# Optimization experiments

Measured on AMD Instinct MI355X. Metric: run time of the kernel, lower is better.

## Reference

```python
import jax, jax.numpy as jnp
import numpy as np

EPS_NORM = 1e-12  # F.normalize default eps
EPS_LN = 1e-6     # LayerNorm eps from module


def setup_inputs() -> dict:
    key = jax.random.key(0)
    ks = jax.random.split(key, 4)
    bs, S, h = 32, 512, 1024
    data = jax.random.normal(ks[0], (bs, S, h), dtype=jnp.float32)
    scale = 1.0 / np.sqrt(h)
    wq = jax.random.normal(ks[1], (h, h), dtype=jnp.float32) * scale
    wk = jax.random.normal(ks[2], (h, h), dtype=jnp.float32) * scale
    wv = jax.random.normal(ks[3], (h, h), dtype=jnp.float32) * scale
    gamma = jnp.ones((h,), dtype=jnp.float32)
    beta = jnp.zeros((h,), dtype=jnp.float32)
    return {"data": data, "wq": wq, "wk": wk, "wv": wv, "gamma": gamma, "beta": beta}


def reference(data, wq, wk, wv, gamma, beta):
    # data: [bs, S, h]; single-head attention, dropout is identity in eval mode
    bs, S, h = data.shape
    temperature = jnp.asarray(h, data.dtype) ** 0.5
    # torch Linear: x @ W^T
    q = jnp.einsum('bsh,dh->bsd', data, wq)
    k = jnp.einsum('bsh,dh->bsd', data, wk)
    v = jnp.einsum('bsh,dh->bsd', data, wv)
    # scaled scores [bs, S, S]
    attn = jnp.einsum('bsd,btd->bst', q / temperature, k)
    # divide by abs of the GLOBAL min over the whole tensor
    attn = attn / jnp.abs(jnp.min(attn))
    # L2-normalize along last dim (F.normalize)
    l2 = jnp.sqrt(jnp.sum(attn * attn, axis=-1, keepdims=True))
    attn = attn / jnp.maximum(l2, EPS_NORM)
    attn = jax.nn.softmax(attn, axis=-1)
    out = jnp.einsum('bst,btd->bsd', attn, v)
    out = out + data  # residual
    # LayerNorm over last dim
    mean = jnp.mean(out, axis=-1, keepdims=True)
    var = jnp.mean((out - mean) ** 2, axis=-1, keepdims=True)
    out = (out - mean) * jax.lax.rsqrt(var + EPS_LN) * gamma + beta
    # concat flattened output [bs, S*h] with flattened attn [bs, S*S]
    return jnp.concatenate((out.reshape(bs, -1), attn.reshape(bs, -1)), axis=1)
```

## Files before the change

### kernel.cpp

```cpp
#include <hip/hip_runtime.h>
#include <hip/hip_bf16.h>


typedef float f32x4 __attribute__((ext_vector_type(4)));
typedef int i32x4v __attribute__((ext_vector_type(4)));
typedef int i32x8v __attribute__((ext_vector_type(8)));

struct alignas(16) US8 { unsigned short s[8]; };
struct alignas(8)  US4 { unsigned short s[4]; };

#define WS_XB   0ull
#define WS_XF8  33554432ull
#define WS_WF8  50331648ull
#define WS_QF8  53477376ull
#define WS_KF8  70254592ull
#define WS_VT8  87031808ull
#define WS_S    103809024ull
#define WS_P8   120586240ull
#define WS_O    128974848ull
#define WS_NEED 162529280ull

__device__ __forceinline__ unsigned short f32_to_bf16(float f) {
  unsigned int u = __builtin_bit_cast(unsigned int, f);
  u += 0x7fffu + ((u >> 16) & 1u);
  return (unsigned short)(u >> 16);
}
__device__ __forceinline__ float bf16_to_f32(unsigned short h) {
  return __builtin_bit_cast(float, (unsigned int)h << 16);
}

__device__ __forceinline__ void gload_lds16(const void* g, void* lds) {
  __builtin_amdgcn_global_load_lds(
      (const __attribute__((address_space(1))) unsigned int*)g,
      (__attribute__((address_space(3))) unsigned int*)lds, 16, 0, 0);
}

__device__ __forceinline__ float wave_sum(float v) {
#pragma unroll
  for (int off = 32; off > 0; off >>= 1) v += __shfl_xor(v, off);
  return v;
}
__device__ __forceinline__ float wave_max(float v) {
#pragma unroll
  for (int off = 32; off > 0; off >>= 1) v = fmaxf(v, __shfl_xor(v, off));
  return v;
}

__device__ __forceinline__ unsigned int pk_fp8x4(float a, float b, float c, float d) {
  unsigned int v = 0;
  v = __builtin_amdgcn_cvt_pk_fp8_f32(a, b, v, false);
  v = __builtin_amdgcn_cvt_pk_fp8_f32(c, d, v, true);
  return v;
}
__device__ __forceinline__ unsigned char f32_to_fp8(float v) {
  return (unsigned char)(__builtin_amdgcn_cvt_pk_fp8_f32(v, v, 0, false) & 0xffu);
}

__global__ __launch_bounds__(256) void cvt_data(const float* __restrict__ src,
                                                unsigned short* __restrict__ dstb,
                                                unsigned int* __restrict__ dst8,
                                                int n8) {
  int i = blockIdx.x * 256 + threadIdx.x;
  if (i >= n8) return;
  const float4* sp = (const float4*)(src + (size_t)i * 8);
  float4 a = sp[0], b = sp[1];
  US8 u;
  u.s[0] = f32_to_bf16(a.x); u.s[1] = f32_to_bf16(a.y);
  u.s[2] = f32_to_bf16(a.z); u.s[3] = f32_to_bf16(a.w);
  u.s[4] = f32_to_bf16(b.x); u.s[5] = f32_to_bf16(b.y);
  u.s[6] = f32_to_bf16(b.z); u.s[7] = f32_to_bf16(b.w);
  *(US8*)(dstb + (size_t)i * 8) = u;
  uint2 w;
  w.x = pk_fp8x4(a.x, a.y, a.z, a.w);
  w.y = pk_fp8x4(b.x, b.y, b.z, b.w);
  *(uint2*)(dst8 + (size_t)i * 2) = w;
}

__global__ __launch_bounds__(256) void cvt_w3(const float* __restrict__ wq,
                                              const float* __restrict__ wk,
                                              const float* __restrict__ wv,
                                              unsigned int* __restrict__ dst8) {
  const int z = blockIdx.y;
  const float* src = (z == 0) ? wq : (z == 1) ? wk : wv;
  int i = blockIdx.x * 256 + threadIdx.x;
  const float4* sp = (const float4*)(src + (size_t)i * 8);
  float4 a = sp[0], b = sp[1];
  uint2 w;
  w.x = pk_fp8x4(a.x, a.y, a.z, a.w);
  w.y = pk_fp8x4(b.x, b.y, b.z, b.w);
  *(uint2*)(dst8 + (size_t)z * 262144 + (size_t)i * 2) = w;
}

template <int KB, int NKT>
__device__ __forceinline__ void f8c128(const char* __restrict__ Ag,
                                       const char* __restrict__ Bg,
                                       char* lds, f32x4 (&acc)[4][4]) {
  const int tid = threadIdx.x;
  const int w = tid >> 6, lane = tid & 63;
  const int wm = w >> 1, wn = w & 1;
  const int lr = lane & 15, lk4 = lane >> 4;

  const int sc = ((tid & 3) ^ ((tid >> 3) & 3)) * 16;
  const char* pA = Ag + (size_t)(tid >> 2) * KB + sc;
  const char* pB = Bg + (size_t)(tid >> 2) * KB + sc;
  const size_t R64 = (size_t)64 * KB;

  const int swz = (lr >> 1) & 3;
  const int c0 = (lk4 & 1) * 2;
  const int cb0 = ((c0) ^ swz) * 16;
  const int cb1 = ((c0 + 1) ^ swz) * 16;
  const int panA = (lk4 >> 1) * 8192;
  const int panB = 16384 + (lk4 >> 1) * 8192;
  const int rowA = (wm * 64 + lr) * 64;
  const int rowB = (wn * 64 + lr) * 64;

#define STAGE8(DD)                                                            \
  do {                                                                        \
    char* dd_ = (DD);                                                         \
    gload_lds16(pA,            dd_ + tid * 16);                               \
    gload_lds16(pA + R64,      dd_ + 4096 + tid * 16);                        \
    gload_lds16(pA + 64,       dd_ + 8192 + tid * 16);                        \
    gload_lds16(pA + R64 + 64, dd_ + 12288 + tid * 16);                       \
    gload_lds16(pB,            dd_ + 16384 + tid * 16);                       \
    gload_lds16(pB + R64,      dd_ + 20480 + tid * 16);                       \
    gload_lds16(pB + 64,       dd_ + 24576 + tid * 16);                       \
    gload_lds16(pB + R64 + 64, dd_ + 28672 + tid * 16);                       \
    pA += 128; pB += 128;                                                     \
  } while (0)

#define MK8(D, OFF)                                                           \
  do {                                                                        \
    i32x4v lo_ = *(const i32x4v*)(sp + (OFF) + cb0);                          \
    i32x4v hi_ = *(const i32x4v*)(sp + (OFF) + cb1);                          \
    D[0] = lo_[0]; D[1] = lo_[1]; D[2] = lo_[2]; D[3] = lo_[3];               \
    D[4] = hi_[0]; D[5] = hi_[1]; D[6] = hi_[2]; D[7] = hi_[3];               \
  } while (0)

#define MFMA128(ACC, AV, BV)                                                  \
  asm("v_mfma_f32_16x16x128_f8f6f4 %0, %1, %2, %0"                            \
      : "+a"(ACC) : "v"(AV), "v"(BV))

  STAGE8(lds);

#pragma unroll
  for (int t = 0; t < NKT; ++t) {
    const int slot = t & 1;
    if (t + 1 < NKT) {
      STAGE8(lds + (slot ^ 1) * 32768);
      asm volatile("s_waitcnt vmcnt(8)" ::: "memory");
    } else {
      asm volatile("s_waitcnt vmcnt(0)" ::: "memory");
    }
    __builtin_amdgcn_s_barrier();
    __builtin_amdgcn_sched_barrier(0);
    const char* sp = lds + slot * 32768;
    i32x8v a0, a1, b0, b1, b2, b3;
    MK8(a0, panA + rowA);          MK8(a1, panA + rowA + 1024);
    MK8(b0, panB + rowB);          MK8(b1, panB + rowB + 1024);
    MK8(b2, panB + rowB + 2048);   MK8(b3, panB + rowB + 3072);
    __builtin_amdgcn_s_setprio(1);
    MFMA128(acc[0][0], a0, b0); MFMA128(acc[0][1], a0, b1);
    MFMA128(acc[0][2], a0, b2); MFMA128(acc[0][3], a0, b3);
    MFMA128(acc[1][0], a1, b0); MFMA128(acc[1][1], a1, b1);
    MFMA128(acc[1][2], a1, b2); MFMA128(acc[1][3], a1, b3);
    __builtin_amdgcn_s_setprio(0);
    i32x8v a2, a3;
    MK8(a2, panA + rowA + 2048);   MK8(a3, panA + rowA + 3072);
    __builtin_amdgcn_s_setprio(1);
    MFMA128(acc[2][0], a2, b0); MFMA128(acc[2][1], a2, b1);
    MFMA128(acc[2][2], a2, b2); MFMA128(acc[2][3], a2, b3);
    MFMA128(acc[3][0], a3, b0); MFMA128(acc[3][1], a3, b1);
    MFMA128(acc[3][2], a3, b2); MFMA128(acc[3][3], a3, b3);
    __builtin_amdgcn_s_setprio(0);
    __builtin_amdgcn_sched_barrier(0);
    __builtin_amdgcn_s_barrier();
  }

#undef MFMA128
#undef MK8
#undef STAGE8
}

__global__ __launch_bounds__(256, 2) void qkv_128(
    const unsigned char* __restrict__ Xf8, const unsigned char* __restrict__ Wf8,
    unsigned char* __restrict__ Qf8, unsigned char* __restrict__ Kf8,
    unsigned char* __restrict__ Vt8) {
  __shared__ alignas(16) char smc[2][32768];
  const int bid = blockIdx.x;
  const int wg = (bid & 7) * 384 + (bid >> 3);
  const int bm = wg / 24, bn = wg % 24;
  const char* Ag = (const char*)Xf8 + (size_t)bm * 128 * 1024;
  const char* Bg = (const char*)Wf8 + (size_t)bn * 128 * 1024;
  f32x4 acc[4][4] = {};
  f8c128<1024, 8>(Ag, Bg, &smc[0][0], acc);

  const int tid = threadIdx.x;
  const int w = tid >> 6, lane = tid & 63;
  const int wm = w >> 1, wn = w & 1;
  const int lr = lane & 15, lk4 = lane >> 4;
  const int cr = lk4 << 2;
  const int z = bn >> 3;
  const int gr0 = bm * 128 + wm * 64;
  const int gc0 = (bn & 7) * 128 + wn * 64;
  if (z < 2) {
    unsigned char* C = (z == 0) ? Qf8 : Kf8;
#pragma unroll
    for (int m = 0; m < 4; ++m)
#pragma unroll
      for (int n = 0; n < 4; ++n)
#pragma unroll
        for (int i = 0; i < 4; ++i)
          C[(size_t)(gr0 + m * 16 + cr + i) * 1024 + (gc0 + n * 16 + lr)] =
              f32_to_fp8(acc[m][n][i]);
  } else {
#pragma unroll
    for (int m = 0; m < 4; ++m) {
      const int gr = gr0 + m * 16 + cr;
      const int b = gr >> 9, tt = gr & 511;
#pragma unroll
      for (int n = 0; n < 4; ++n) {
        const int d = gc0 + n * 16 + lr;
        unsigned int u = pk_fp8x4(acc[m][n][0], acc[m][n][1],
                                  acc[m][n][2], acc[m][n][3]);
        *(unsigned int*)(Vt8 + ((size_t)b * 1024 + d) * 512 + tt) = u;
      }
    }
  }
}

__global__ __launch_bounds__(256, 2) void s_f8(
    const unsigned char* __restrict__ Qf8, const unsigned char* __restrict__ Kf8,
    unsigned short* __restrict__ S) {
  __shared__ alignas(16) char smc[2][32768];
  const int bn = blockIdx.x, bm = blockIdx.y, b = blockIdx.z;
  const char* Ag = (const char*)Qf8 + ((size_t)b * 512 + bm * 128) * 1024;
  const char* Bg = (const char*)Kf8 + ((size_t)b * 512 + bn * 128) * 1024;
  f32x4 acc[4][4] = {};
  f8c128<1024, 8>(Ag, Bg, &smc[0][0], acc);

  const int tid = threadIdx.x;
  const int w = tid >> 6, lane = tid & 63;
  const int wm = w >> 1, wn = w & 1;
  const int lr = lane & 15, lk4 = lane >> 4;
  const int cr = lk4 << 2;
  unsigned short* Cp = S + (size_t)b * 262144;
  const int rbase = bm * 128 + wm * 64;
  const int cbase = bn * 128 + wn * 64;
#pragma unroll
  for (int m = 0; m < 4; ++m)
#pragma unroll
    for (int n = 0; n < 4; ++n)
#pragma unroll
      for (int i = 0; i < 4; ++i)
        Cp[(size_t)(rbase + m * 16 + cr + i) * 512 + (cbase + n * 16 + lr)] =
            f32_to_bf16(acc[m][n][i]);
}

__global__ __launch_bounds__(256) void softmax_rows(const unsigned short* __restrict__ S,
                                                    float* __restrict__ out,
                                                    unsigned char* __restrict__ P8) {
  const int w = threadIdx.x >> 6, lane = threadIdx.x & 63;
  const int r = blockIdx.x * 4 + w;
  const int b = r >> 9, s = r & 511;
  US8 v = *(const US8*)(S + (size_t)r * 512 + lane * 8);
  float x[8];
#pragma unroll
  for (int i = 0; i < 8; ++i) x[i] = bf16_to_f32(v.s[i]);
  float ss = 0.f;
#pragma unroll
  for (int i = 0; i < 8; ++i) ss += x[i] * x[i];
  ss = wave_sum(ss);
  const float inv = 1.0f / fmaxf(sqrtf(ss), 1e-12f);
  float mx = -1e30f;
#pragma unroll
  for (int i = 0; i < 8; ++i) { x[i] *= inv; mx = fmaxf(mx, x[i]); }
  mx = wave_max(mx);
  float se = 0.f;
#pragma unroll
  for (int i = 0; i < 8; ++i) { x[i] = __expf(x[i] - mx); se += x[i]; }
  se = wave_sum(se);
  const float rs = 1.0f / se;
#pragma unroll
  for (int i = 0; i < 8; ++i) x[i] *= rs;

  float* op = out + (size_t)b * 786432 + 524288 + (size_t)s * 512 + lane * 8;
  float4 o0 = {x[0], x[1], x[2], x[3]};
  float4 o1 = {x[4], x[5], x[6], x[7]};
  *(float4*)op = o0;
  *(float4*)(op + 4) = o1;
  uint2 pw;
  pw.x = pk_fp8x4(x[0] * 256.f, x[1] * 256.f, x[2] * 256.f, x[3] * 256.f);
  pw.y = pk_fp8x4(x[4] * 256.f, x[5] * 256.f, x[6] * 256.f, x[7] * 256.f);
  *(uint2*)(P8 + (size_t)r * 512 + lane * 8) = pw;
}

__global__ __launch_bounds__(256, 2) void pv_f8(
    const unsigned char* __restrict__ P8, const unsigned char* __restrict__ Vt8,
    unsigned short* __restrict__ O) {
  __shared__ alignas(16) char smc[2][32768];
  const int bn = blockIdx.x, bm = blockIdx.y, b = blockIdx.z;
  const char* Ag = (const char*)P8 + ((size_t)b * 512 + bm * 128) * 512;
  const char* Bg = (const char*)Vt8 + ((size_t)b * 1024 + bn * 128) * 512;
  f32x4 acc[4][4] = {};
  f8c128<512, 4>(Ag, Bg, &smc[0][0], acc);

  const int tid = threadIdx.x;
  const int w = tid >> 6, lane = tid & 63;
  const int wm = w >> 1, wn = w & 1;
  const int lr = lane & 15, lk4 = lane >> 4;
  const int cr = lk4 << 2;
  const int grow = b * 512 + bm * 128 + wm * 64;
  const int cbase = bn * 128 + wn * 64;
#pragma unroll
  for (int m = 0; m < 4; ++m)
#pragma unroll
    for (int n = 0; n < 4; ++n)
#pragma unroll
      for (int i = 0; i < 4; ++i)
        O[(size_t)(grow + m * 16 + cr + i) * 1024 + (cbase + n * 16 + lr)] =
            f32_to_bf16(acc[m][n][i] * 0.00390625f);
}

__global__ __launch_bounds__(256) void ln_rows(const unsigned short* __restrict__ O,
                                               const unsigned short* __restrict__ Xb,
                                               const float* __restrict__ gamma,
                                               const float* __restrict__ beta,
                                               float* __restrict__ out) {
  const int w = threadIdx.x >> 6, lane = threadIdx.x & 63;
  const int r = blockIdx.x * 4 + w;
  const int b = r >> 9, s = r & 511;
  const unsigned short* orow = O + (size_t)r * 1024;
  const unsigned short* drow = Xb + (size_t)r * 1024;
  float x[16];
  float sm = 0.f, sq = 0.f;
#pragma unroll
  for (int j = 0; j < 4; ++j) {
    const int col = j * 256 + lane * 4;
    US4 o4 = *(const US4*)(orow + col);
    US4 d4 = *(const US4*)(drow + col);
    x[j * 4 + 0] = bf16_to_f32(o4.s[0]) + bf16_to_f32(d4.s[0]);
    x[j * 4 + 1] = bf16_to_f32(o4.s[1]) + bf16_to_f32(d4.s[1]);
    x[j * 4 + 2] = bf16_to_f32(o4.s[2]) + bf16_to_f32(d4.s[2]);
    x[j * 4 + 3] = bf16_to_f32(o4.s[3]) + bf16_to_f32(d4.s[3]);
  }
#pragma unroll
  for (int i = 0; i < 16; ++i) { sm += x[i]; sq += x[i] * x[i]; }
  sm = wave_sum(sm);
  sq = wave_sum(sq);
  const float mean = sm * (1.0f / 1024.0f);
  const float var = sq * (1.0f / 1024.0f) - mean * mean;
  const float rstd = rsqrtf(var + 1e-6f);
  float* op = out + (size_t)b * 786432 + (size_t)s * 1024;
#pragma unroll
  for (int j = 0; j < 4; ++j) {
    const int col = j * 256 + lane * 4;
    float4 g4 = *(const float4*)(gamma + col);
    float4 b4 = *(const float4*)(beta + col);
    float4 y;
    y.x = (x[j * 4 + 0] - mean) * rstd * g4.x + b4.x;
    y.y = (x[j * 4 + 1] - mean) * rstd * g4.y + b4.y;
    y.z = (x[j * 4 + 2] - mean) * rstd * g4.z + b4.z;
    y.w = (x[j * 4 + 3] - mean) * rstd * g4.w + b4.w;
    *(float4*)(op + col) = y;
  }
}

extern "C" void kernel_launch(void* const* d_in, const int* in_sizes, int n_in,
                              void* d_out, int out_size, void* d_ws, size_t ws_size,
                              hipStream_t stream) {
  const float* data  = (const float*)d_in[0];
  const float* wq    = (const float*)d_in[1];
  const float* wk    = (const float*)d_in[2];
  const float* wv    = (const float*)d_in[3];
  const float* gamma = (const float*)d_in[4];
  const float* beta  = (const float*)d_in[5];
  float* out = (float*)d_out;
  char* ws = (char*)d_ws;
  if (ws_size < WS_NEED) return;

  unsigned short* Xb  = (unsigned short*)(ws + WS_XB);
  unsigned int*   Xf8 = (unsigned int*)(ws + WS_XF8);
  unsigned int*   Wf8 = (unsigned int*)(ws + WS_WF8);
  unsigned char*  Qf8 = (unsigned char*)(ws + WS_QF8);
  unsigned char*  Kf8 = (unsigned char*)(ws + WS_KF8);
  unsigned char*  Vt8 = (unsigned char*)(ws + WS_VT8);
  unsigned short* S   = (unsigned short*)(ws + WS_S);
  unsigned char*  P8  = (unsigned char*)(ws + WS_P8);
  unsigned short* O   = (unsigned short*)(ws + WS_O);

  cvt_data<<<8192, 256, 0, stream>>>(data, Xb, Xf8, 2097152);
  cvt_w3<<<dim3(512, 3), 256, 0, stream>>>(wq, wk, wv, Wf8);
  qkv_128<<<3072, 256, 0, stream>>>((const unsigned char*)Xf8,
                                    (const unsigned char*)Wf8, Qf8, Kf8, Vt8);
  s_f8<<<dim3(4, 4, 32), 256, 0, stream>>>(Qf8, Kf8, S);
  softmax_rows<<<4096, 256, 0, stream>>>(S, out, P8);
  pv_f8<<<dim3(8, 4, 32), 256, 0, stream>>>(P8, Vt8, O);
  ln_rows<<<4096, 256, 0, stream>>>(O, Xb, gamma, beta, out);
}
```

Measured before the change: 163.7 us.

## Use 256x256 QKV GEMM tiles, merge conversion kernels, widen LayerNorm loads

```diff
diff --git a/kernel.cpp b/kernel.cpp
--- a/kernel.cpp
+++ b/kernel.cpp
@@ -56,39 +56,166 @@
   return (unsigned char)(__builtin_amdgcn_cvt_pk_fp8_f32(v, v, 0, false) & 0xffu);
 }
 
-__global__ __launch_bounds__(256) void cvt_data(const float* __restrict__ src,
-                                                unsigned short* __restrict__ dstb,
-                                                unsigned int* __restrict__ dst8,
-                                                int n8) {
-  int i = blockIdx.x * 256 + threadIdx.x;
-  if (i >= n8) return;
-  const float4* sp = (const float4*)(src + (size_t)i * 8);
-  float4 a = sp[0], b = sp[1];
-  US8 u;
-  u.s[0] = f32_to_bf16(a.x); u.s[1] = f32_to_bf16(a.y);
-  u.s[2] = f32_to_bf16(a.z); u.s[3] = f32_to_bf16(a.w);
-  u.s[4] = f32_to_bf16(b.x); u.s[5] = f32_to_bf16(b.y);
-  u.s[6] = f32_to_bf16(b.z); u.s[7] = f32_to_bf16(b.w);
-  *(US8*)(dstb + (size_t)i * 8) = u;
-  uint2 w;
-  w.x = pk_fp8x4(a.x, a.y, a.z, a.w);
-  w.y = pk_fp8x4(b.x, b.y, b.z, b.w);
-  *(uint2*)(dst8 + (size_t)i * 2) = w;
-}
-
-__global__ __launch_bounds__(256) void cvt_w3(const float* __restrict__ wq,
-                                              const float* __restrict__ wk,
-                                              const float* __restrict__ wv,
-                                              unsigned int* __restrict__ dst8) {
-  const int z = blockIdx.y;
-  const float* src = (z == 0) ? wq : (z == 1) ? wk : wv;
-  int i = blockIdx.x * 256 + threadIdx.x;
-  const float4* sp = (const float4*)(src + (size_t)i * 8);
-  float4 a = sp[0], b = sp[1];
-  uint2 w;
-  w.x = pk_fp8x4(a.x, a.y, a.z, a.w);
-  w.y = pk_fp8x4(b.x, b.y, b.z, b.w);
-  *(uint2*)(dst8 + (size_t)z * 262144 + (size_t)i * 2) = w;
+__global__ __launch_bounds__(256) void cvt_all(const float* __restrict__ data,
+                                               const float* __restrict__ wq,
+                                               const float* __restrict__ wk,
+                                               const float* __restrict__ wv,
+                                               unsigned short* __restrict__ Xb,
+                                               unsigned int* __restrict__ Xf8,
+                                               unsigned int* __restrict__ Wf8) {
+  const int bid = blockIdx.x;
+  if (bid < 8192) {
+    int i = bid * 256 + threadIdx.x;
+    const float4* sp = (const float4*)(data + (size_t)i * 8);
+    float4 a = sp[0], b = sp[1];
+    US8 u;
+    u.s[0] = f32_to_bf16(a.x); u.s[1] = f32_to_bf16(a.y);
+    u.s[2] = f32_to_bf16(a.z); u.s[3] = f32_to_bf16(a.w);
+    u.s[4] = f32_to_bf16(b.x); u.s[5] = f32_to_bf16(b.y);
+    u.s[6] = f32_to_bf16(b.z); u.s[7] = f32_to_bf16(b.w);
+    *(US8*)(Xb + (size_t)i * 8) = u;
+    uint2 w;
+    w.x = pk_fp8x4(a.x, a.y, a.z, a.w);
+    w.y = pk_fp8x4(b.x, b.y, b.z, b.w);
+    *(uint2*)(Xf8 + (size_t)i * 2) = w;
+  } else {
+    const int r = bid - 8192;
+    const int z = r >> 9;
+    const float* src = (z == 0) ? wq : (z == 1) ? wk : wv;
+    int i = (r & 511) * 256 + threadIdx.x;
+    const float4* sp = (const float4*)(src + (size_t)i * 8);
+    float4 a = sp[0], b = sp[1];
+    uint2 w;
+    w.x = pk_fp8x4(a.x, a.y, a.z, a.w);
+    w.y = pk_fp8x4(b.x, b.y, b.z, b.w);
+    *(uint2*)(Wf8 + (size_t)z * 262144 + (size_t)i * 2) = w;
+  }
+}
+
+__global__ __launch_bounds__(512, 2) void qkv_256(
+    const unsigned char* __restrict__ Xf8, const unsigned char* __restrict__ Wf8,
+    unsigned char* __restrict__ Qf8, unsigned char* __restrict__ Kf8,
+    unsigned char* __restrict__ Vt8) {
+  __shared__ alignas(16) char smc[2][65536];
+
+  const int tid = threadIdx.x;
+  const int w = tid >> 6, lane = tid & 63;
+  const int wm = w >> 2, wn = w & 3;
+  const int lr = lane & 15, lk4 = lane >> 4;
+
+  const int bid = blockIdx.x;
+  const int wg = (bid & 7) * 96 + (bid >> 3);
+  const int bm = wg / 12, bn = wg % 12;
+
+  const char* Ag = (const char*)Xf8 + (size_t)bm * 256 * 1024;
+  const char* Bg = (const char*)Wf8 + (size_t)bn * 256 * 1024;
+
+  const int sc = ((tid & 3) ^ ((tid >> 3) & 3)) * 16;
+  const char* pA = Ag + (size_t)(tid >> 2) * 1024 + sc;
+  const char* pB = Bg + (size_t)(tid >> 2) * 1024 + sc;
+
+  const int swz = (lr >> 1) & 3;
+  const int c0 = (lk4 & 1) * 2;
+  const int cb0 = ((c0) ^ swz) * 16;
+  const int cb1 = ((c0 + 1) ^ swz) * 16;
+  const int panA = (lk4 >> 1) * 16384;
+  const int panB = 32768 + (lk4 >> 1) * 16384;
+  const int rowA = (wm * 128 + lr) * 64;
+  const int rowB = (wn * 64 + lr) * 64;
+
+  f32x4 acc[8][4] = {};
+
+#define STAGE8(DD)                                                            \
+  do {                                                                        \
+    char* dd_ = (DD);                                                         \
+    gload_lds16(pA,                dd_ + tid * 16);                           \
+    gload_lds16(pA + 131072,       dd_ + 8192 + tid * 16);                    \
+    gload_lds16(pA + 64,           dd_ + 16384 + tid * 16);                   \
+    gload_lds16(pA + 131072 + 64,  dd_ + 24576 + tid * 16);                   \
+    gload_lds16(pB,                dd_ + 32768 + tid * 16);                   \
+    gload_lds16(pB + 131072,       dd_ + 40960 + tid * 16);                   \
+    gload_lds16(pB + 64,           dd_ + 49152 + tid * 16);                   \
+    gload_lds16(pB + 131072 + 64,  dd_ + 57344 + tid * 16);                   \
+    pA += 128; pB += 128;                                                     \
+  } while (0)
+
+#define MK8(D, OFF)                                                           \
+  do {                                                                        \
+    i32x4v lo_ = *(const i32x4v*)(sp + (OFF) + cb0);                          \
+    i32x4v hi_ = *(const i32x4v*)(sp + (OFF) + cb1);                          \
+    D[0] = lo_[0]; D[1] = lo_[1]; D[2] = lo_[2]; D[3] = lo_[3];               \
+    D[4] = hi_[0]; D[5] = hi_[1]; D[6] = hi_[2]; D[7] = hi_[3];               \
+  } while (0)
+
+#define MFMA128(ACC, AV, BV)                                                  \
+  asm("v_mfma_f32_16x16x128_f8f6f4 %0, %1, %2, %0"                            \
+      : "+a"(ACC) : "v"(AV), "v"(BV))
+
+  STAGE8(smc[0]);
+
+#pragma unroll
+  for (int t = 0; t < 8; ++t) {
+    const int slot = t & 1;
+    if (t + 1 < 8) {
+      STAGE8(smc[slot ^ 1]);
+      asm volatile("s_waitcnt vmcnt(8)" ::: "memory");
+    } else {
+      asm volatile("s_waitcnt vmcnt(0)" ::: "memory");
+    }
+    __builtin_amdgcn_s_barrier();
+    __builtin_amdgcn_sched_barrier(0);
+    const char* sp = smc[slot];
+    i32x8v b0, b1, b2, b3;
+    MK8(b0, panB + rowB);          MK8(b1, panB + rowB + 1024);
+    MK8(b2, panB + rowB + 2048);   MK8(b3, panB + rowB + 3072);
+#pragma unroll
+    for (int mb = 0; mb < 8; mb += 2) {
+      i32x8v a0, a1;
+      MK8(a0, panA + rowA + mb * 1024);
+      MK8(a1, panA + rowA + (mb + 1) * 1024);
+      __builtin_amdgcn_s_setprio(1);
+      MFMA128(acc[mb][0], a0, b0);     MFMA128(acc[mb][1], a0, b1);
+      MFMA128(acc[mb][2], a0, b2);     MFMA128(acc[mb][3], a0, b3);
+      MFMA128(acc[mb + 1][0], a1, b0); MFMA128(acc[mb + 1][1], a1, b1);
+      MFMA128(acc[mb + 1][2], a1, b2); MFMA128(acc[mb + 1][3], a1, b3);
+      __builtin_amdgcn_s_setprio(0);
+    }
+    __builtin_amdgcn_sched_barrier(0);
+    __builtin_amdgcn_s_barrier();
+  }
+
+#undef MFMA128
+#undef MK8
+#undef STAGE8
+
+  const int cr = lk4 << 2;
+  const int z = bn >> 2;
+  const int gr0 = bm * 256 + wm * 128;
+  const int gc0 = (bn & 3) * 256 + wn * 64;
+  if (z < 2) {
+    unsigned char* C = (z == 0) ? Qf8 : Kf8;
+#pragma unroll
+    for (int m = 0; m < 8; ++m)
+#pragma unroll
+      for (int n = 0; n < 4; ++n)
+#pragma unroll
+        for (int i = 0; i < 4; ++i)
+          C[(size_t)(gr0 + m * 16 + cr + i) * 1024 + (gc0 + n * 16 + lr)] =
+              f32_to_fp8(acc[m][n][i]);
+  } else {
+#pragma unroll
+    for (int m = 0; m < 8; ++m) {
+      const int gr = gr0 + m * 16 + cr;
+      const int b = gr >> 9, tt = gr & 511;
+#pragma unroll
+      for (int n = 0; n < 4; ++n) {
+        const int d = gc0 + n * 16 + lr;
+        unsigned int u = pk_fp8x4(acc[m][n][0], acc[m][n][1],
+                                  acc[m][n][2], acc[m][n][3]);
+        *(unsigned int*)(Vt8 + ((size_t)b * 1024 + d) * 512 + tt) = u;
+      }
+    }
+  }
 }
 
 template <int KB, int NKT>
@@ -181,53 +308,6 @@
 #undef STAGE8
 }
 
-__global__ __launch_bounds__(256, 2) void qkv_128(
-    const unsigned char* __restrict__ Xf8, const unsigned char* __restrict__ Wf8,
-    unsigned char* __restrict__ Qf8, unsigned char* __restrict__ Kf8,
-    unsigned char* __restrict__ Vt8) {
-  __shared__ alignas(16) char smc[2][32768];
-  const int bid = blockIdx.x;
-  const int wg = (bid & 7) * 384 + (bid >> 3);
-  const int bm = wg / 24, bn = wg % 24;
-  const char* Ag = (const char*)Xf8 + (size_t)bm * 128 * 1024;
-  const char* Bg = (const char*)Wf8 + (size_t)bn * 128 * 1024;
-  f32x4 acc[4][4] = {};
-  f8c128<1024, 8>(Ag, Bg, &smc[0][0], acc);
-
-  const int tid = threadIdx.x;
-  const int w = tid >> 6, lane = tid & 63;
-  const int wm = w >> 1, wn = w & 1;
-  const int lr = lane & 15, lk4 = lane >> 4;
-  const int cr = lk4 << 2;
-  const int z = bn >> 3;
-  const int gr0 = bm * 128 + wm * 64;
-  const int gc0 = (bn & 7) * 128 + wn * 64;
-  if (z < 2) {
-    unsigned char* C = (z == 0) ? Qf8 : Kf8;
-#pragma unroll
-    for (int m = 0; m < 4; ++m)
-#pragma unroll
-      for (int n = 0; n < 4; ++n)
-#pragma unroll
-        for (int i = 0; i < 4; ++i)
-          C[(size_t)(gr0 + m * 16 + cr + i) * 1024 + (gc0 + n * 16 + lr)] =
-              f32_to_fp8(acc[m][n][i]);
-  } else {
-#pragma unroll
-    for (int m = 0; m < 4; ++m) {
-      const int gr = gr0 + m * 16 + cr;
-      const int b = gr >> 9, tt = gr & 511;
-#pragma unroll
-      for (int n = 0; n < 4; ++n) {
-        const int d = gc0 + n * 16 + lr;
-        unsigned int u = pk_fp8x4(acc[m][n][0], acc[m][n][1],
-                                  acc[m][n][2], acc[m][n][3]);
-        *(unsigned int*)(Vt8 + ((size_t)b * 1024 + d) * 512 + tt) = u;
-      }
-    }
-  }
-}
-
 __global__ __launch_bounds__(256, 2) void s_f8(
     const unsigned char* __restrict__ Qf8, const unsigned char* __restrict__ Kf8,
     unsigned short* __restrict__ S) {
@@ -334,14 +414,13 @@
   float x[16];
   float sm = 0.f, sq = 0.f;
 #pragma unroll
-  for (int j = 0; j < 4; ++j) {
-    const int col = j * 256 + lane * 4;
-    US4 o4 = *(const US4*)(orow + col);
-    US4 d4 = *(const US4*)(drow + col);
-    x[j * 4 + 0] = bf16_to_f32(o4.s[0]) + bf16_to_f32(d4.s[0]);
-    x[j * 4 + 1] = bf16_to_f32(o4.s[1]) + bf16_to_f32(d4.s[1]);
-    x[j * 4 + 2] = bf16_to_f32(o4.s[2]) + bf16_to_f32(d4.s[2]);
-    x[j * 4 + 3] = bf16_to_f32(o4.s[3]) + bf16_to_f32(d4.s[3]);
+  for (int j = 0; j < 2; ++j) {
+    const int col = j * 512 + lane * 8;
+    US8 o8 = *(const US8*)(orow + col);
+    US8 d8 = *(const US8*)(drow + col);
+#pragma unroll
+    for (int k = 0; k < 8; ++k)
+      x[j * 8 + k] = bf16_to_f32(o8.s[k]) + bf16_to_f32(d8.s[k]);
   }
 #pragma unroll
   for (int i = 0; i < 16; ++i) { sm += x[i]; sq += x[i] * x[i]; }
@@ -352,16 +431,23 @@
   const float rstd = rsqrtf(var + 1e-6f);
   float* op = out + (size_t)b * 786432 + (size_t)s * 1024;
 #pragma unroll
-  for (int j = 0; j < 4; ++j) {
-    const int col = j * 256 + lane * 4;
-    float4 g4 = *(const float4*)(gamma + col);
-    float4 b4 = *(const float4*)(beta + col);
-    float4 y;
-    y.x = (x[j * 4 + 0] - mean) * rstd * g4.x + b4.x;
-    y.y = (x[j * 4 + 1] - mean) * rstd * g4.y + b4.y;
-    y.z = (x[j * 4 + 2] - mean) * rstd * g4.z + b4.z;
-    y.w = (x[j * 4 + 3] - mean) * rstd * g4.w + b4.w;
-    *(float4*)(op + col) = y;
+  for (int j = 0; j < 2; ++j) {
+    const int col = j * 512 + lane * 8;
+    float4 g0 = *(const float4*)(gamma + col);
+    float4 g1 = *(const float4*)(gamma + col + 4);
+    float4 b0 = *(const float4*)(beta + col);
+    float4 b1 = *(const float4*)(beta + col + 4);
+    float4 y0, y1;
+    y0.x = (x[j * 8 + 0] - mean) * rstd * g0.x + b0.x;
+    y0.y = (x[j * 8 + 1] - mean) * rstd * g0.y + b0.y;
+    y0.z = (x[j * 8 + 2] - mean) * rstd * g0.z + b0.z;
+    y0.w = (x[j * 8 + 3] - mean) * rstd * g0.w + b0.w;
+    y1.x = (x[j * 8 + 4] - mean) * rstd * g1.x + b1.x;
+    y1.y = (x[j * 8 + 5] - mean) * rstd * g1.y + b1.y;
+    y1.z = (x[j * 8 + 6] - mean) * rstd * g1.z + b1.z;
+    y1.w = (x[j * 8 + 7] - mean) * rstd * g1.w + b1.w;
+    *(float4*)(op + col) = y0;
+    *(float4*)(op + col + 4) = y1;
   }
 }
 
@@ -388,10 +474,9 @@
   unsigned char*  P8  = (unsigned char*)(ws + WS_P8);
   unsigned short* O   = (unsigned short*)(ws + WS_O);
 
-  cvt_data<<<8192, 256, 0, stream>>>(data, Xb, Xf8, 2097152);
-  cvt_w3<<<dim3(512, 3), 256, 0, stream>>>(wq, wk, wv, Wf8);
-  qkv_128<<<3072, 256, 0, stream>>>((const unsigned char*)Xf8,
-                                    (const unsigned char*)Wf8, Qf8, Kf8, Vt8);
+  cvt_all<<<9728, 256, 0, stream>>>(data, wq, wk, wv, Xb, Xf8, Wf8);
+  qkv_256<<<768, 512, 0, stream>>>((const unsigned char*)Xf8,
+                                   (const unsigned char*)Wf8, Qf8, Kf8, Vt8);
   s_f8<<<dim3(4, 4, 32), 256, 0, stream>>>(Qf8, Kf8, S);
   softmax_rows<<<4096, 256, 0, stream>>>(S, out, P8);
   pv_f8<<<dim3(8, 4, 32), 256, 0, stream>>>(P8, Vt8, O);
```

New measurement: 170.7 us. +4.3%, slower.
